# Optimization experiments

Measured on AMD Instinct MI355X. Metric: run time of the kernel, lower is better.

## Reference

```python
import jax, jax.numpy as jnp
import numpy as np

N = 10000; E = 160000; C = 32; NB = 128; H = 64; L = 3; NL = 4; RC = 5.0
DIMS = [1, 3, 5, 7]

def _sph(v):
    # real spherical harmonics l=0..3 of unit vectors v [E,3]
    x, y, z = v[:, 0], v[:, 1], v[:, 2]
    s3 = 3.0 ** 0.5; s5 = 5.0 ** 0.5; s15 = 15.0 ** 0.5; s7 = 7.0 ** 0.5
    sh0 = jnp.ones_like(x)[:, None]
    sh1 = s3 * v
    sh2 = jnp.stack([s15 * x * y, s15 * y * z, (s5 / 2) * (3 * z * z - 1),
                     s15 * x * z, (s15 / 2) * (x * x - y * y)], -1)
    c1 = (35.0 / 8) ** 0.5; c2 = 105.0 ** 0.5; c3 = (21.0 / 8) ** 0.5; c4 = s7 / 2; c5 = (105.0 ** 0.5) / 2
    sh3 = jnp.stack([c1 * y * (3 * x * x - y * y), c2 * x * y * z, c3 * y * (5 * z * z - 1),
                     c4 * (5 * z ** 3 - 3 * z), c3 * x * (5 * z * z - 1),
                     c5 * z * (x * x - y * y), c1 * x * (x * x - 3 * y * y)], -1)
    return [sh0, sh1, sh2, sh3]

def setup_inputs() -> dict:
    key = jax.random.key(0)
    ks = jax.random.split(key, 14)
    inp = {}
    inp['pos'] = jax.random.uniform(ks[0], (N, 3), jnp.float32) * 10.0  # box of side 10
    inp['node_embed'] = jax.random.normal(ks[1], (4, C), jnp.float32)
    inp['rw1'] = jax.random.normal(ks[2], (NB, H), jnp.float32) * 0.1
    inp['rb1'] = jax.random.normal(ks[3], (H,), jnp.float32) * 0.1
    inp['rw2'] = jax.random.normal(ks[4], (H, L * NL * C), jnp.float32) * 0.1
    inp['rb2'] = jax.random.normal(ks[5], (L * NL * C,), jnp.float32) * 0.1
    inp['self_w'] = jax.random.normal(ks[6], (L, NL, C, C), jnp.float32) * (1.0 / C ** 0.5)
    inp['msg_w'] = jax.random.normal(ks[7], (L, NL, C, C), jnp.float32) * (1.0 / C ** 0.5)
    inp['gate_w'] = jax.random.normal(ks[8], (L, C, C), jnp.float32) * (1.0 / C ** 0.5)
    inp['edge_w'] = jax.random.normal(ks[9], (H, NL * C), jnp.float32) * 0.1
    inp['edge_b'] = jax.random.normal(ks[10], (NL * C,), jnp.float32) * 0.1
    inp['species'] = jax.random.randint(ks[11], (N,), 0, 4)
    inp['edge_index'] = jax.random.randint(ks[12], (2, E), 0, N)
    return inp

def reference(pos, node_embed, rw1, rb1, rw2, rb2, self_w, msg_w, gate_w,
              edge_w, edge_b, species, edge_index):
    src, dst = edge_index[0], edge_index[1]
    vec = pos[dst] - pos[src]                       # [E,3]
    r = jnp.sqrt(jnp.sum(vec * vec, -1) + 1e-12)    # [E]
    u = jnp.clip(r / RC, 0.0, 1.0)
    env = 0.5 * (jnp.cos(jnp.pi * u) + 1.0)         # smooth cutoff, 0 beyond rc
    n = jnp.arange(1, NB + 1, dtype=pos.dtype)
    rb = env[:, None] * (2.0 / RC) ** 0.5 * jnp.sin(jnp.pi * n * u[:, None]) / r[:, None]  # Bessel basis [E,NB]
    h = jax.nn.silu(rb @ rw1 + rb1)                 # [E,H]
    w_all = (h @ rw2 + rb2).reshape(E, L, NL, C)    # per-layer per-l radial weights
    ew = (h @ edge_w + edge_b).reshape(E, NL, C)
    sh = _sph(vec / r[:, None])                     # list of [E, 2l+1]
    # node features per l: [N, C, 2l+1]; l=0 initialized from species embedding
    f = [node_embed[species][:, :, None]] + [jnp.zeros((N, C, d), pos.dtype) for d in DIMS[1:]]
    for t in range(L):
        s = f[0][src][:, :, 0]                      # sender scalars [E,C]
        new = []
        for l in range(NL):
            # scalar-gated radial x SH message (equivariant): [E,C,2l+1]
            m = w_all[:, t, l, :, None] * s[:, :, None] * sh[l][:, None, :]
            agg = jax.ops.segment_sum(m, dst, num_segments=N)
            new.append(jnp.einsum('ncm,cd->ndm', f[l], self_w[t, l]) +
                       jnp.einsum('ncm,cd->ndm', agg, msg_w[t, l]))
        gate = jax.nn.sigmoid(new[0][:, :, 0] @ gate_w[t])  # [N,C]
        f = [jax.nn.silu(new[0])] + [new[l] * gate[:, :, None] for l in range(1, NL)]
    node_out = jnp.concatenate([f[l].reshape(N, C * DIMS[l]) for l in range(NL)], -1)   # [N,512]
    g = f[0][src][:, :, 0] + f[0][dst][:, :, 0]     # [E,C]
    edge_out = jnp.concatenate(
        [(ew[:, l, :, None] * g[:, :, None] * sh[l][:, None, :]).reshape(E, C * DIMS[l])
         for l in range(NL)], -1)                   # [E,512]
    return jnp.concatenate([node_out, edge_out], 0)  # [N+E, 512]
```

## Files before the change

### kernel.cpp

```cpp
#include <hip/hip_runtime.h>

#define NN 10000
#define EE 160000
#define CC 32
#define NBAS 128
#define HH 64
#define LL 3
#define ECH 80000

__device__ __forceinline__ float sigmoidf_(float x) { return 1.0f / (1.0f + expf(-x)); }

__device__ __forceinline__ void edge_geom(const float* pos, int src, int dst,
                                          float& inv_r, float& u, float& pref,
                                          float& x, float& y, float& z) {
    float vx = pos[dst * 3 + 0] - pos[src * 3 + 0];
    float vy = pos[dst * 3 + 1] - pos[src * 3 + 1];
    float vz = pos[dst * 3 + 2] - pos[src * 3 + 2];
    float r2 = vx * vx + vy * vy + vz * vz + 1e-12f;
    float r = sqrtf(r2);
    inv_r = 1.0f / r;
    u = fminf(r * 0.2f, 1.0f);
    const float PI = 3.14159265358979f;
    float env = 0.5f * (cosf(PI * u) + 1.0f);
    pref = env * 0.6324555320336759f * inv_r;
    x = vx * inv_r; y = vy * inv_r; z = vz * inv_r;
}

__device__ __forceinline__ void sph_all(float x, float y, float z, float* shv) {
    const float s3 = 1.7320508075688772f, s5 = 2.23606797749979f, s15 = 3.872983346207417f;
    const float c1 = 2.0916500663351885f;
    const float c2 = 10.246950765959598f;
    const float c3 = 1.6201851746019649f;
    const float c4 = 1.3228756555322954f;
    const float c5 = 5.123475382979799f;
    shv[0] = 1.0f;
    shv[1] = s3 * x; shv[2] = s3 * y; shv[3] = s3 * z;
    shv[4] = s15 * x * y;
    shv[5] = s15 * y * z;
    shv[6] = 0.5f * s5 * (3.0f * z * z - 1.0f);
    shv[7] = s15 * x * z;
    shv[8] = 0.5f * s15 * (x * x - y * y);
    shv[9]  = c1 * y * (3.0f * x * x - y * y);
    shv[10] = c2 * x * y * z;
    shv[11] = c3 * y * (5.0f * z * z - 1.0f);
    shv[12] = c4 * (5.0f * z * z * z - 3.0f * z);
    shv[13] = c3 * x * (5.0f * z * z - 1.0f);
    shv[14] = c5 * z * (x * x - y * y);
    shv[15] = c1 * x * (x * x - 3.0f * y * y);
}

__global__ void k_deg(const int* __restrict__ ei, int* __restrict__ deg) {
    int e = blockIdx.x * blockDim.x + threadIdx.x;
    if (e < EE) atomicAdd(&deg[ei[EE + e]], 1);
}

__global__ __launch_bounds__(256) void k_scan(const int* __restrict__ deg, int* __restrict__ rowptr) {
    __shared__ int part[256];
    const int CHUNK = 40;
    int tid = threadIdx.x;
    int s = 0;
#pragma unroll
    for (int k = 0; k < CHUNK; k++) {
        int idx = tid * CHUNK + k;
        if (idx < NN) s += deg[idx];
    }
    part[tid] = s;
    __syncthreads();
    for (int off = 1; off < 256; off <<= 1) {
        int v = (tid >= off) ? part[tid - off] : 0;
        __syncthreads();
        part[tid] += v;
        __syncthreads();
    }
    int run = (tid > 0) ? part[tid - 1] : 0;
#pragma unroll
    for (int k = 0; k < CHUNK; k++) {
        int idx = tid * CHUNK + k;
        if (idx < NN) { rowptr[idx] = run; run += deg[idx]; }
    }
    if (tid == 255) rowptr[NN] = run;
}

__global__ void k_scatter(const int* __restrict__ ei, const int* __restrict__ rowptr,
                          int* __restrict__ cursor, int* __restrict__ csr) {
    int e = blockIdx.x * blockDim.x + threadIdx.x;
    if (e >= EE) return;
    int d = ei[EE + e];
    int slot = atomicAdd(&cursor[d], 1);
    csr[rowptr[d] + slot] = e;
}

__global__ void k_init_f(const float* __restrict__ ne, const int* __restrict__ species,
                         float* __restrict__ f, float* __restrict__ f0) {
    int idx = blockIdx.x * blockDim.x + threadIdx.x;
    if (idx >= NN * CC * 16) return;
    int m = idx & 15;
    int c = (idx >> 4) & 31;
    int n = idx >> 9;
    float v = (m == 0) ? ne[species[n] * CC + c] : 0.0f;
    f[idx] = v;
    if (m == 0) f0[n * CC + c] = v;
}

__global__ __launch_bounds__(256) void k_edge_pre(
    const float* __restrict__ pos, const float* __restrict__ rw1, const float* __restrict__ rb1,
    const int* __restrict__ ei, float* __restrict__ hbuf, float* __restrict__ shbuf) {
    __shared__ float rw1_s[NBAS * HH];
    __shared__ float rb_s[4][NBAS];
    int tid = threadIdx.x;
    for (int i = tid; i < NBAS * HH; i += 256) rw1_s[i] = rw1[i];
    int w = tid >> 6, lane = tid & 63;
    int e = blockIdx.x * 4 + w;
    int src = ei[e], dst = ei[EE + e];
    float inv_r, u, pref, x, y, z;
    edge_geom(pos, src, dst, inv_r, u, pref, x, y, z);
    const float PI = 3.14159265358979f;
#pragma unroll
    for (int rep = 0; rep < 2; rep++) {
        int k = lane + rep * 64;
        rb_s[w][k] = pref * sinf(PI * (float)(k + 1) * u);
    }
    float shv[16];
    sph_all(x, y, z, shv);
    if (lane < 16) {
        float v = shv[0];
#pragma unroll
        for (int k = 1; k < 16; k++) v = (lane == k) ? shv[k] : v;
        shbuf[e * 16 + lane] = v;
    }
    __syncthreads();
    float acc = rb1[lane];
#pragma unroll 8
    for (int n = 0; n < NBAS; n++) acc += rb_s[w][n] * rw1_s[n * HH + lane];
    acc = acc * sigmoidf_(acc);
    hbuf[e * HH + lane] = acc;
}

template<int MODE>
__global__ __launch_bounds__(256) void k_gemm(
    const float* __restrict__ hbuf, const float* __restrict__ W,
    int wstride, int wcol, const float* __restrict__ bias,
    const float* __restrict__ f0, const int* __restrict__ ei,
    const int* __restrict__ csr, float* __restrict__ outw, int ebase) {
    __shared__ float w_s[HH * 128];
    __shared__ float h_s[64][68];
    __shared__ int e_s[64];
    int tid = threadIdx.x;
    int kbase = blockIdx.x * 64 + ebase;
    for (int i = tid; i < HH * 32; i += 256) {
        int j = i >> 5, o4 = (i & 31) << 2;
        *(float4*)&w_s[j * 128 + o4] = *(const float4*)&W[(size_t)j * wstride + wcol + o4];
    }
    {
        int r = tid >> 2, q = tid & 3;
        int p = kbase + r;
        int e = (MODE == 0) ? csr[p] : p;
        if (q == 0) e_s[r] = e;
        const float4* hp = (const float4*)(hbuf + (size_t)e * HH + q * 16);
        float4 v0 = hp[0], v1 = hp[1], v2 = hp[2], v3 = hp[3];
        float4* dp = (float4*)&h_s[r][q * 16];
        dp[0] = v0; dp[1] = v1; dp[2] = v2; dp[3] = v3;
    }
    __syncthreads();
    int ob = (tid & 31) << 2;
    int r0 = (tid >> 5) << 3;
    float acc[8][4];
#pragma unroll
    for (int i = 0; i < 8; i++) { acc[i][0] = 0.f; acc[i][1] = 0.f; acc[i][2] = 0.f; acc[i][3] = 0.f; }
#pragma unroll 2
    for (int k0 = 0; k0 < HH; k0 += 4) {
        float4 w0 = *(float4*)&w_s[(k0 + 0) * 128 + ob];
        float4 w1 = *(float4*)&w_s[(k0 + 1) * 128 + ob];
        float4 w2 = *(float4*)&w_s[(k0 + 2) * 128 + ob];
        float4 w3 = *(float4*)&w_s[(k0 + 3) * 128 + ob];
#pragma unroll
        for (int i = 0; i < 8; i++) {
            float4 hv = *(float4*)&h_s[r0 + i][k0];
            acc[i][0] += hv.x * w0.x; acc[i][1] += hv.x * w0.y; acc[i][2] += hv.x * w0.z; acc[i][3] += hv.x * w0.w;
            acc[i][0] += hv.y * w1.x; acc[i][1] += hv.y * w1.y; acc[i][2] += hv.y * w1.z; acc[i][3] += hv.y * w1.w;
            acc[i][0] += hv.z * w2.x; acc[i][1] += hv.z * w2.y; acc[i][2] += hv.z * w2.z; acc[i][3] += hv.z * w2.w;
            acc[i][0] += hv.w * w3.x; acc[i][1] += hv.w * w3.y; acc[i][2] += hv.w * w3.z; acc[i][3] += hv.w * w3.w;
        }
    }
    float4 bv = *(const float4*)&bias[wcol + ob];
    int cc = ob & 31;
#pragma unroll
    for (int i = 0; i < 8; i++) {
        int rr = r0 + i;
        int e = e_s[rr];
        float4 sc;
        if (MODE == 0) {
            int src = ei[e];
            sc = *(const float4*)&f0[src * CC + cc];
        } else {
            int src = ei[e], dst = ei[EE + e];
            float4 s1 = *(const float4*)&f0[src * CC + cc];
            float4 s2 = *(const float4*)&f0[dst * CC + cc];
            sc.x = s1.x + s2.x; sc.y = s1.y + s2.y; sc.z = s1.z + s2.z; sc.w = s1.w + s2.w;
        }
        float4 res;
        res.x = (acc[i][0] + bv.x) * sc.x;
        res.y = (acc[i][1] + bv.y) * sc.y;
        res.z = (acc[i][2] + bv.z) * sc.z;
        res.w = (acc[i][3] + bv.w) * sc.w;
        size_t prow = (size_t)(kbase - ebase + rr);
        *(float4*)&outw[prow * 128 + ob] = res;
    }
}

__global__ __launch_bounds__(256) void k_agg2(
    const float* __restrict__ aw, const float* __restrict__ shbuf,
    const int* __restrict__ rowptr, const int* __restrict__ csr,
    float* __restrict__ agg) {
    int w = threadIdx.x >> 6, lane = threadIdx.x & 63;
    int n = blockIdx.x * 4 + w;
    int c = lane & 31;
    int half = lane >> 5;
    float acc0[3] = {0.f, 0.f, 0.f};
    float acc1[7] = {0.f, 0.f, 0.f, 0.f, 0.f, 0.f, 0.f};
    int beg = rowptr[n], end = rowptr[n + 1];
    for (int k = beg; k < end; k++) {
        int e = csr[k];
        float a0 = aw[(size_t)k * 128 + lane];
        float a1 = aw[(size_t)k * 128 + 64 + lane];
        const float4* shp = (const float4*)(shbuf + (size_t)e * 16);
        float4 s0 = shp[0], s1 = shp[1], s2 = shp[2], s3 = shp[3];
        if (half == 0) {
            acc0[0] += a0 * s0.x;
            acc1[0] += a1 * s1.x; acc1[1] += a1 * s1.y; acc1[2] += a1 * s1.z; acc1[3] += a1 * s1.w;
            acc1[4] += a1 * s2.x;
        } else {
            acc0[0] += a0 * s0.y; acc0[1] += a0 * s0.z; acc0[2] += a0 * s0.w;
            acc1[0] += a1 * s2.y; acc1[1] += a1 * s2.z; acc1[2] += a1 * s2.w;
            acc1[3] += a1 * s3.x; acc1[4] += a1 * s3.y; acc1[5] += a1 * s3.z; acc1[6] += a1 * s3.w;
        }
    }
    int l0 = half, dl0 = 2 * l0 + 1, mo0 = l0 * l0;
    int l1 = 2 + half, dl1 = 2 * l1 + 1, mo1 = l1 * l1;
    float* ap = agg + ((size_t)n * CC + c) * 16;
#pragma unroll
    for (int m = 0; m < 3; m++)
        if (m < dl0) ap[mo0 + m] = acc0[m];
#pragma unroll
    for (int m = 0; m < 7; m++)
        if (m < dl1) ap[mo1 + m] = acc1[m];
}

__global__ __launch_bounds__(256) void k_node(
    const float* __restrict__ f_cur, const float* __restrict__ agg,
    const float* __restrict__ self_w, const float* __restrict__ msg_w,
    const float* __restrict__ gate_w, float* __restrict__ f_next,
    float* __restrict__ f0_out, int t) {
    __shared__ float new_s[4][CC * 16];
    __shared__ float gate_s[4][CC];
    int w = threadIdx.x >> 6, lane = threadIdx.x & 63;
    int n = blockIdx.x * 4 + w;
    int d = lane & 31, mg = lane >> 5;
#pragma unroll
    for (int k = 0; k < 8; k++) {
        int m = mg + 2 * k;
        int l = (m == 0) ? 0 : (m < 4) ? 1 : (m < 9) ? 2 : 3;
        const float* sw = self_w + (size_t)((t * 4 + l) * CC) * CC + d;
        const float* mw = msg_w + (size_t)((t * 4 + l) * CC) * CC + d;
        const float* fp = f_cur + (size_t)n * CC * 16 + m;
        const float* ap = agg + (size_t)n * CC * 16 + m;
        float acc = 0.0f;
#pragma unroll 8
        for (int c = 0; c < CC; c++)
            acc += fp[c * 16] * sw[c * CC] + ap[c * 16] * mw[c * CC];
        new_s[w][d * 16 + m] = acc;
    }
    __syncthreads();
    if (mg == 0) {
        float g = 0.0f;
#pragma unroll 8
        for (int c = 0; c < CC; c++) g += new_s[w][c * 16 + 0] * gate_w[((size_t)t * CC + c) * CC + d];
        gate_s[w][d] = sigmoidf_(g);
    }
    __syncthreads();
#pragma unroll
    for (int k = 0; k < 8; k++) {
        int m = mg + 2 * k;
        float v = new_s[w][d * 16 + m];
        if (m == 0) v = v * sigmoidf_(v);
        else v *= gate_s[w][d];
        f_next[((size_t)n * CC + d) * 16 + m] = v;
        if (m == 0) f0_out[n * CC + d] = v;
    }
}

__global__ void k_out_node(const float* __restrict__ f, float* __restrict__ out) {
    int idx = blockIdx.x * blockDim.x + threadIdx.x;
    if (idx >= NN * 512) return;
    int n = idx >> 9, q = idx & 511;
    int l, c, m;
    if (q < 32) { l = 0; c = q; m = 0; }
    else if (q < 128) { l = 1; c = (q - 32) / 3; m = (q - 32) % 3; }
    else if (q < 288) { l = 2; c = (q - 128) / 5; m = (q - 128) % 5; }
    else { l = 3; c = (q - 288) / 7; m = (q - 288) % 7; }
    out[idx] = f[((size_t)n * CC + c) * 16 + l * l + m];
}

__global__ __launch_bounds__(256) void k_out_edge2(
    const float* __restrict__ eaw, const float* __restrict__ shbuf,
    float* __restrict__ out, int ebase) {
    int w = threadIdx.x >> 6, lane = threadIdx.x & 63;
    int eloc = blockIdx.x * 4 + w;
    int e = ebase + eloc;
    int c = lane & 31;
    float a0 = eaw[(size_t)eloc * 128 + lane];
    float a1 = eaw[(size_t)eloc * 128 + 64 + lane];
    const float4* shp = (const float4*)(shbuf + (size_t)e * 16);
    float4 s0 = shp[0], s1 = shp[1], s2 = shp[2], s3 = shp[3];
    size_t orow = ((size_t)NN + e) * 512;
    if (lane < 32) {
        out[orow + c] = a0 * s0.x;
        float* op = &out[orow + 128 + c * 5];
        op[0] = a1 * s1.x; op[1] = a1 * s1.y; op[2] = a1 * s1.z; op[3] = a1 * s1.w;
        op[4] = a1 * s2.x;
    } else {
        float* op0 = &out[orow + 32 + c * 3];
        op0[0] = a0 * s0.y; op0[1] = a0 * s0.z; op0[2] = a0 * s0.w;
        float* op1 = &out[orow + 288 + c * 7];
        op1[0] = a1 * s2.y; op1[1] = a1 * s2.z; op1[2] = a1 * s2.w;
        op1[3] = a1 * s3.x; op1[4] = a1 * s3.y; op1[5] = a1 * s3.z; op1[6] = a1 * s3.w;
    }
}

__global__ __launch_bounds__(256) void k_out_edge(
    const float* __restrict__ pos, const float* __restrict__ rw1, const float* __restrict__ rb1,
    const float* __restrict__ edge_w, const float* __restrict__ edge_b,
    const float* __restrict__ f0, const int* __restrict__ ei, float* __restrict__ out) {
    __shared__ float rw1_s[NBAS * HH];
    __shared__ float ew_s[HH * 128];
    __shared__ float rb_s[4][NBAS];
    __shared__ float h_s[4][HH];
    __shared__ float g_s[4][CC];
    __shared__ float sh_s[4][16];
    int tid = threadIdx.x;
    for (int i = tid; i < NBAS * HH; i += 256) rw1_s[i] = rw1[i];
    for (int i = tid; i < HH * 128; i += 256) ew_s[i] = edge_w[i];
    int w = tid >> 6, lane = tid & 63;
    int e = blockIdx.x * 4 + w;
    int src = ei[e], dst = ei[EE + e];
    float inv_r, u, pref, x, y, z;
    edge_geom(pos, src, dst, inv_r, u, pref, x, y, z);
    const float PI = 3.14159265358979f;
#pragma unroll
    for (int rep = 0; rep < 2; rep++) {
        int k = lane + rep * 64;
        rb_s[w][k] = pref * sinf(PI * (float)(k + 1) * u);
    }
    float shv[16];
    sph_all(x, y, z, shv);
    if (lane < 16) {
        float v = shv[0];
#pragma unroll
        for (int k = 1; k < 16; k++) v = (lane == k) ? shv[k] : v;
        sh_s[w][lane] = v;
    }
    if (lane < CC) g_s[w][lane] = f0[src * CC + lane] + f0[dst * CC + lane];
    __syncthreads();
    float acc = rb1[lane];
#pragma unroll 8
    for (int n = 0; n < NBAS; n++) acc += rb_s[w][n] * rw1_s[n * HH + lane];
    h_s[w][lane] = acc * sigmoidf_(acc);
    __syncthreads();
    size_t orow = ((size_t)NN + e) * 512;
#pragma unroll
    for (int rep = 0; rep < 2; rep++) {
        int o = lane + rep * 64;
        int l = o >> 5, c = o & 31;
        float a = edge_b[o];
#pragma unroll 8
        for (int j = 0; j < HH; j++) a += h_s[w][j] * ew_s[j * 128 + o];
        float base = a * g_s[w][c];
        int dl = 2 * l + 1, mo = l * l, co = 32 * l * l;
        for (int m = 0; m < dl; m++) out[orow + co + c * dl + m] = base * sh_s[w][mo + m];
    }
}

extern "C" void kernel_launch(void* const* d_in, const int* in_sizes, int n_in,
                              void* d_out, int out_size, void* d_ws, size_t ws_size,
                              hipStream_t stream) {
    const float* pos        = (const float*)d_in[0];
    const float* node_embed = (const float*)d_in[1];
    const float* rw1        = (const float*)d_in[2];
    const float* rb1        = (const float*)d_in[3];
    const float* rw2        = (const float*)d_in[4];
    const float* rb2        = (const float*)d_in[5];
    const float* self_w     = (const float*)d_in[6];
    const float* msg_w      = (const float*)d_in[7];
    const float* gate_w     = (const float*)d_in[8];
    const float* edge_w     = (const float*)d_in[9];
    const float* edge_b     = (const float*)d_in[10];
    const int* species      = (const int*)d_in[11];
    const int* ei           = (const int*)d_in[12];
    float* out = (float*)d_out;

    float* f0fin = (float*)d_ws;
    float* f0ar  = f0fin + (size_t)NN * CC;
    float* hbuf  = f0ar + (size_t)NN * CC;
    float* shbuf = hbuf + (size_t)EE * HH;
    float* fA    = shbuf + (size_t)EE * 16;
    float* agg   = fA + (size_t)NN * 512;
    int* deg     = (int*)(agg + (size_t)NN * 512);
    int* rowptr  = deg + NN;
    int* cursor  = rowptr + NN + 1;
    int* csr     = cursor + NN;
    size_t base_need = (size_t)((char*)(csr + EE) - (char*)d_ws);
    size_t extra_need = ((size_t)NN * 512 + (size_t)EE * 128) * 4;
    float* fB;
    float* aw;
    bool deep_fallback = false;
    if (ws_size >= base_need + extra_need) {
        fB = (float*)((char*)d_ws + base_need);
        aw = fB + (size_t)NN * 512;
    } else if (ws_size >= base_need) {
        fB = out + (size_t)NN * 512;
        aw = fB + (size_t)NN * 512;
    } else {
        deep_fallback = true;
        float* s = out + (size_t)NN * 512;
        hbuf = s; shbuf = hbuf + (size_t)EE * HH;
        fA = shbuf + (size_t)EE * 16;
        agg = fA + (size_t)NN * 512;
        fB = agg + (size_t)NN * 512;
        aw = fB + (size_t)NN * 512;
        deg = (int*)(aw + (size_t)EE * 128);
        rowptr = deg + NN; cursor = rowptr + NN + 1; csr = cursor + NN;
    }
    float* eaw = fA;

    hipMemsetAsync(deg, 0, (size_t)NN * 4, stream);
    hipMemsetAsync(cursor, 0, (size_t)NN * 4, stream);
    k_deg<<<(EE + 255) / 256, 256, 0, stream>>>(ei, deg);
    k_scan<<<1, 256, 0, stream>>>(deg, rowptr);
    k_scatter<<<(EE + 255) / 256, 256, 0, stream>>>(ei, rowptr, cursor, csr);

    k_init_f<<<(NN * CC * 16 + 255) / 256, 256, 0, stream>>>(node_embed, species, fA, f0ar);
    k_edge_pre<<<EE / 4, 256, 0, stream>>>(pos, rw1, rb1, ei, hbuf, shbuf);

    float* fc = fA;
    float* fn = fB;
    for (int t = 0; t < LL; t++) {
        k_gemm<0><<<EE / 64, 256, 0, stream>>>(hbuf, rw2, 384, t * 128, rb2, f0ar, ei, csr, aw, 0);
        k_agg2<<<NN / 4, 256, 0, stream>>>(aw, shbuf, rowptr, csr, agg);
        float* f0o = (t == LL - 1) ? f0fin : f0ar;
        k_node<<<NN / 4, 256, 0, stream>>>(fc, agg, self_w, msg_w, gate_w, fn, f0o, t);
        float* tmp = fc; fc = fn; fn = tmp;
    }

    k_out_node<<<(NN * 512 + 255) / 256, 256, 0, stream>>>(fc, out);
    if (!deep_fallback) {
        for (int cb = 0; cb < EE; cb += ECH) {
            k_gemm<1><<<ECH / 64, 256, 0, stream>>>(hbuf, edge_w, 128, 0, edge_b, f0fin, ei, csr, eaw, cb);
            k_out_edge2<<<ECH / 4, 256, 0, stream>>>(eaw, shbuf, out, cb);
        }
    } else {
        k_out_edge<<<EE / 4, 256, 0, stream>>>(pos, rw1, rb1, edge_w, edge_b, f0fin, ei, out);
    }
}
```

Before: 1.194 ms.

## Batch radial GEMMs across layers, tile edge MLP, and fuse edge output

The first radial MLP layer becomes a 64-edge tiled GEMM, and the sine basis is computed with a Chebyshev recurrence instead of one sinf per basis term. The per-layer rw2 GEMM is hoisted into a single launch that computes all three layers' weights, which are stored in a wider buffer. The sender-scalar multiply moves into the aggregation kernel. The edge-output GEMM and the spherical-harmonic expansion are fused into one kernel that writes vectorized outputs. This removes repeated weight and hbuf passes and intermediate round trips, at the cost of a larger workspace and extra gather loads in aggregation.

```diff
diff --git a/kernel.cpp b/kernel.cpp
--- a/kernel.cpp
+++ b/kernel.cpp
@@ -6,7 +6,6 @@
 #define NBAS 128
 #define HH 64
 #define LL 3
-#define ECH 80000
 
 __device__ __forceinline__ float sigmoidf_(float x) { return 1.0f / (1.0f + expf(-x)); }
 
@@ -106,112 +105,137 @@
     const float* __restrict__ pos, const float* __restrict__ rw1, const float* __restrict__ rb1,
     const int* __restrict__ ei, float* __restrict__ hbuf, float* __restrict__ shbuf) {
     __shared__ float rw1_s[NBAS * HH];
-    __shared__ float rb_s[4][NBAS];
+    __shared__ float rb_s[64 * 132];
     int tid = threadIdx.x;
-    for (int i = tid; i < NBAS * HH; i += 256) rw1_s[i] = rw1[i];
-    int w = tid >> 6, lane = tid & 63;
-    int e = blockIdx.x * 4 + w;
-    int src = ei[e], dst = ei[EE + e];
-    float inv_r, u, pref, x, y, z;
-    edge_geom(pos, src, dst, inv_r, u, pref, x, y, z);
-    const float PI = 3.14159265358979f;
-#pragma unroll
-    for (int rep = 0; rep < 2; rep++) {
-        int k = lane + rep * 64;
-        rb_s[w][k] = pref * sinf(PI * (float)(k + 1) * u);
-    }
-    float shv[16];
-    sph_all(x, y, z, shv);
-    if (lane < 16) {
-        float v = shv[0];
-#pragma unroll
-        for (int k = 1; k < 16; k++) v = (lane == k) ? shv[k] : v;
-        shbuf[e * 16 + lane] = v;
-    }
-    __syncthreads();
-    float acc = rb1[lane];
-#pragma unroll 8
-    for (int n = 0; n < NBAS; n++) acc += rb_s[w][n] * rw1_s[n * HH + lane];
-    acc = acc * sigmoidf_(acc);
-    hbuf[e * HH + lane] = acc;
-}
-
-template<int MODE>
-__global__ __launch_bounds__(256) void k_gemm(
-    const float* __restrict__ hbuf, const float* __restrict__ W,
-    int wstride, int wcol, const float* __restrict__ bias,
-    const float* __restrict__ f0, const int* __restrict__ ei,
-    const int* __restrict__ csr, float* __restrict__ outw, int ebase) {
+    int ebase = blockIdx.x * 64;
+    for (int i = tid; i < NBAS * HH / 4; i += 256)
+        *(float4*)&rw1_s[i * 4] = *(const float4*)&rw1[i * 4];
+    {
+        int r = tid >> 2, q = tid & 3;
+        int e = ebase + r;
+        int src = ei[e], dst = ei[EE + e];
+        float inv_r, u, pref, x, y, z;
+        edge_geom(pos, src, dst, inv_r, u, pref, x, y, z);
+        float shv[16];
+        sph_all(x, y, z, shv);
+        float4 sv;
+        sv.x = shv[q * 4 + 0]; sv.y = shv[q * 4 + 1];
+        sv.z = shv[q * 4 + 2]; sv.w = shv[q * 4 + 3];
+        *(float4*)&shbuf[(size_t)e * 16 + q * 4] = sv;
+        const float PI = 3.14159265358979f;
+        float th = PI * u;
+        float tc = 2.0f * cosf(th);
+        int n0 = 32 * q + 1;
+        float sp2 = sinf(th * (float)n0);
+        float sp1 = sinf(th * (float)(n0 + 1));
+        float* rp = &rb_s[r * 132 + 32 * q];
+        float4 v;
+        v.x = pref * sp2; v.y = pref * sp1;
+#pragma unroll
+        for (int j = 2; j < 32; j++) {
+            float s = tc * sp1 - sp2;
+            sp2 = sp1; sp1 = s;
+            float pv = pref * s;
+            int m = j & 3;
+            if (m == 0) v.x = pv;
+            else if (m == 1) v.y = pv;
+            else if (m == 2) v.z = pv;
+            else { v.w = pv; *(float4*)&rp[j - 3] = v; }
+        }
+    }
+    __syncthreads();
+    int col0 = (tid & 15) * 4;
+    int r0 = (tid >> 4) * 4;
+    float acc[4][4];
+#pragma unroll
+    for (int i = 0; i < 4; i++) { acc[i][0] = 0.f; acc[i][1] = 0.f; acc[i][2] = 0.f; acc[i][3] = 0.f; }
+#pragma unroll 2
+    for (int k0 = 0; k0 < NBAS; k0 += 4) {
+        float4 w0 = *(float4*)&rw1_s[(k0 + 0) * HH + col0];
+        float4 w1 = *(float4*)&rw1_s[(k0 + 1) * HH + col0];
+        float4 w2 = *(float4*)&rw1_s[(k0 + 2) * HH + col0];
+        float4 w3 = *(float4*)&rw1_s[(k0 + 3) * HH + col0];
+#pragma unroll
+        for (int i = 0; i < 4; i++) {
+            float4 rv = *(float4*)&rb_s[(r0 + i) * 132 + k0];
+            acc[i][0] += rv.x * w0.x; acc[i][1] += rv.x * w0.y; acc[i][2] += rv.x * w0.z; acc[i][3] += rv.x * w0.w;
+            acc[i][0] += rv.y * w1.x; acc[i][1] += rv.y * w1.y; acc[i][2] += rv.y * w1.z; acc[i][3] += rv.y * w1.w;
+            acc[i][0] += rv.z * w2.x; acc[i][1] += rv.z * w2.y; acc[i][2] += rv.z * w2.z; acc[i][3] += rv.z * w2.w;
+            acc[i][0] += rv.w * w3.x; acc[i][1] += rv.w * w3.y; acc[i][2] += rv.w * w3.z; acc[i][3] += rv.w * w3.w;
+        }
+    }
+    float4 bv = *(const float4*)&rb1[col0];
+#pragma unroll
+    for (int i = 0; i < 4; i++) {
+        float a0 = acc[i][0] + bv.x, a1 = acc[i][1] + bv.y;
+        float a2 = acc[i][2] + bv.z, a3 = acc[i][3] + bv.w;
+        float4 hres;
+        hres.x = a0 * sigmoidf_(a0); hres.y = a1 * sigmoidf_(a1);
+        hres.z = a2 * sigmoidf_(a2); hres.w = a3 * sigmoidf_(a3);
+        *(float4*)&hbuf[(size_t)(ebase + r0 + i) * HH + col0] = hres;
+    }
+}
+
+__global__ __launch_bounds__(256) void k_gemm_all(
+    const float* __restrict__ hbuf, const float* __restrict__ rw2,
+    const float* __restrict__ rb2, const int* __restrict__ csr,
+    float* __restrict__ aw, int panel0, int npanel, int ostride) {
     __shared__ float w_s[HH * 128];
     __shared__ float h_s[64][68];
-    __shared__ int e_s[64];
     int tid = threadIdx.x;
-    int kbase = blockIdx.x * 64 + ebase;
-    for (int i = tid; i < HH * 32; i += 256) {
-        int j = i >> 5, o4 = (i & 31) << 2;
-        *(float4*)&w_s[j * 128 + o4] = *(const float4*)&W[(size_t)j * wstride + wcol + o4];
-    }
+    int pbase = blockIdx.x * 64;
     {
         int r = tid >> 2, q = tid & 3;
-        int p = kbase + r;
-        int e = (MODE == 0) ? csr[p] : p;
-        if (q == 0) e_s[r] = e;
+        int e = csr[pbase + r];
         const float4* hp = (const float4*)(hbuf + (size_t)e * HH + q * 16);
         float4 v0 = hp[0], v1 = hp[1], v2 = hp[2], v3 = hp[3];
         float4* dp = (float4*)&h_s[r][q * 16];
         dp[0] = v0; dp[1] = v1; dp[2] = v2; dp[3] = v3;
     }
-    __syncthreads();
     int ob = (tid & 31) << 2;
     int r0 = (tid >> 5) << 3;
-    float acc[8][4];
-#pragma unroll
-    for (int i = 0; i < 8; i++) { acc[i][0] = 0.f; acc[i][1] = 0.f; acc[i][2] = 0.f; acc[i][3] = 0.f; }
+    for (int p = 0; p < npanel; p++) {
+        int wcol = (panel0 + p) * 128;
+        __syncthreads();
+        for (int i = tid; i < HH * 32; i += 256) {
+            int j = i >> 5, o4 = (i & 31) << 2;
+            *(float4*)&w_s[j * 128 + o4] = *(const float4*)&rw2[(size_t)j * 384 + wcol + o4];
+        }
+        __syncthreads();
+        float acc[8][4];
+#pragma unroll
+        for (int i = 0; i < 8; i++) { acc[i][0] = 0.f; acc[i][1] = 0.f; acc[i][2] = 0.f; acc[i][3] = 0.f; }
 #pragma unroll 2
-    for (int k0 = 0; k0 < HH; k0 += 4) {
-        float4 w0 = *(float4*)&w_s[(k0 + 0) * 128 + ob];
-        float4 w1 = *(float4*)&w_s[(k0 + 1) * 128 + ob];
-        float4 w2 = *(float4*)&w_s[(k0 + 2) * 128 + ob];
-        float4 w3 = *(float4*)&w_s[(k0 + 3) * 128 + ob];
+        for (int k0 = 0; k0 < HH; k0 += 4) {
+            float4 w0 = *(float4*)&w_s[(k0 + 0) * 128 + ob];
+            float4 w1 = *(float4*)&w_s[(k0 + 1) * 128 + ob];
+            float4 w2 = *(float4*)&w_s[(k0 + 2) * 128 + ob];
+            float4 w3 = *(float4*)&w_s[(k0 + 3) * 128 + ob];
+#pragma unroll
+            for (int i = 0; i < 8; i++) {
+                float4 hv = *(float4*)&h_s[r0 + i][k0];
+                acc[i][0] += hv.x * w0.x; acc[i][1] += hv.x * w0.y; acc[i][2] += hv.x * w0.z; acc[i][3] += hv.x * w0.w;
+                acc[i][0] += hv.y * w1.x; acc[i][1] += hv.y * w1.y; acc[i][2] += hv.y * w1.z; acc[i][3] += hv.y * w1.w;
+                acc[i][0] += hv.z * w2.x; acc[i][1] += hv.z * w2.y; acc[i][2] += hv.z * w2.z; acc[i][3] += hv.z * w2.w;
+                acc[i][0] += hv.w * w3.x; acc[i][1] += hv.w * w3.y; acc[i][2] += hv.w * w3.z; acc[i][3] += hv.w * w3.w;
+            }
+        }
+        float4 bv = *(const float4*)&rb2[wcol + ob];
 #pragma unroll
         for (int i = 0; i < 8; i++) {
-            float4 hv = *(float4*)&h_s[r0 + i][k0];
-            acc[i][0] += hv.x * w0.x; acc[i][1] += hv.x * w0.y; acc[i][2] += hv.x * w0.z; acc[i][3] += hv.x * w0.w;
-            acc[i][0] += hv.y * w1.x; acc[i][1] += hv.y * w1.y; acc[i][2] += hv.y * w1.z; acc[i][3] += hv.y * w1.w;
-            acc[i][0] += hv.z * w2.x; acc[i][1] += hv.z * w2.y; acc[i][2] += hv.z * w2.z; acc[i][3] += hv.z * w2.w;
-            acc[i][0] += hv.w * w3.x; acc[i][1] += hv.w * w3.y; acc[i][2] += hv.w * w3.z; acc[i][3] += hv.w * w3.w;
-        }
-    }
-    float4 bv = *(const float4*)&bias[wcol + ob];
-    int cc = ob & 31;
-#pragma unroll
-    for (int i = 0; i < 8; i++) {
-        int rr = r0 + i;
-        int e = e_s[rr];
-        float4 sc;
-        if (MODE == 0) {
-            int src = ei[e];
-            sc = *(const float4*)&f0[src * CC + cc];
-        } else {
-            int src = ei[e], dst = ei[EE + e];
-            float4 s1 = *(const float4*)&f0[src * CC + cc];
-            float4 s2 = *(const float4*)&f0[dst * CC + cc];
-            sc.x = s1.x + s2.x; sc.y = s1.y + s2.y; sc.z = s1.z + s2.z; sc.w = s1.w + s2.w;
-        }
-        float4 res;
-        res.x = (acc[i][0] + bv.x) * sc.x;
-        res.y = (acc[i][1] + bv.y) * sc.y;
-        res.z = (acc[i][2] + bv.z) * sc.z;
-        res.w = (acc[i][3] + bv.w) * sc.w;
-        size_t prow = (size_t)(kbase - ebase + rr);
-        *(float4*)&outw[prow * 128 + ob] = res;
+            float4 res;
+            res.x = acc[i][0] + bv.x; res.y = acc[i][1] + bv.y;
+            res.z = acc[i][2] + bv.z; res.w = acc[i][3] + bv.w;
+            *(float4*)&aw[(size_t)(pbase + r0 + i) * ostride + p * 128 + ob] = res;
+        }
     }
 }
 
 __global__ __launch_bounds__(256) void k_agg2(
     const float* __restrict__ aw, const float* __restrict__ shbuf,
+    const float* __restrict__ f0, const int* __restrict__ ei,
     const int* __restrict__ rowptr, const int* __restrict__ csr,
-    float* __restrict__ agg) {
+    float* __restrict__ agg, int coloff, int ostride) {
     int w = threadIdx.x >> 6, lane = threadIdx.x & 63;
     int n = blockIdx.x * 4 + w;
     int c = lane & 31;
@@ -221,8 +245,10 @@
     int beg = rowptr[n], end = rowptr[n + 1];
     for (int k = beg; k < end; k++) {
         int e = csr[k];
-        float a0 = aw[(size_t)k * 128 + lane];
-        float a1 = aw[(size_t)k * 128 + 64 + lane];
+        int src = ei[e];
+        float fs = f0[src * CC + c];
+        float a0 = aw[(size_t)k * ostride + coloff + lane] * fs;
+        float a1 = aw[(size_t)k * ostride + coloff + 64 + lane] * fs;
         const float4* shp = (const float4*)(shbuf + (size_t)e * 16);
         float4 s0 = shp[0], s1 = shp[1], s2 = shp[2], s3 = shp[3];
         if (half == 0) {
@@ -301,29 +327,84 @@
     out[idx] = f[((size_t)n * CC + c) * 16 + l * l + m];
 }
 
-__global__ __launch_bounds__(256) void k_out_edge2(
-    const float* __restrict__ eaw, const float* __restrict__ shbuf,
-    float* __restrict__ out, int ebase) {
-    int w = threadIdx.x >> 6, lane = threadIdx.x & 63;
-    int eloc = blockIdx.x * 4 + w;
-    int e = ebase + eloc;
-    int c = lane & 31;
-    float a0 = eaw[(size_t)eloc * 128 + lane];
-    float a1 = eaw[(size_t)eloc * 128 + 64 + lane];
-    const float4* shp = (const float4*)(shbuf + (size_t)e * 16);
-    float4 s0 = shp[0], s1 = shp[1], s2 = shp[2], s3 = shp[3];
-    size_t orow = ((size_t)NN + e) * 512;
-    if (lane < 32) {
-        out[orow + c] = a0 * s0.x;
-        float* op = &out[orow + 128 + c * 5];
-        op[0] = a1 * s1.x; op[1] = a1 * s1.y; op[2] = a1 * s1.z; op[3] = a1 * s1.w;
-        op[4] = a1 * s2.x;
-    } else {
-        float* op0 = &out[orow + 32 + c * 3];
-        op0[0] = a0 * s0.y; op0[1] = a0 * s0.z; op0[2] = a0 * s0.w;
-        float* op1 = &out[orow + 288 + c * 7];
-        op1[0] = a1 * s2.y; op1[1] = a1 * s2.z; op1[2] = a1 * s2.w;
-        op1[3] = a1 * s3.x; op1[4] = a1 * s3.y; op1[5] = a1 * s3.z; op1[6] = a1 * s3.w;
+template<int DL>
+__device__ __forceinline__ void emit_edge(float* outp, const float* shp,
+                                          float e0, float e1, float e2, float e3) {
+    float ew[4] = {e0, e1, e2, e3};
+    float buf[4 * DL];
+#pragma unroll
+    for (int cc = 0; cc < 4; cc++)
+#pragma unroll
+        for (int m = 0; m < DL; m++) buf[cc * DL + m] = ew[cc] * shp[m];
+#pragma unroll
+    for (int t = 0; t < DL; t++) *(float4*)&outp[t * 4] = *(float4*)&buf[t * 4];
+}
+
+__global__ __launch_bounds__(256) void k_edge_out(
+    const float* __restrict__ hbuf, const float* __restrict__ shbuf,
+    const float* __restrict__ edge_w, const float* __restrict__ edge_b,
+    const float* __restrict__ f0, const int* __restrict__ ei,
+    float* __restrict__ out) {
+    __shared__ float w_s[HH * 128];
+    __shared__ float h_s[64][68];
+    __shared__ float sh_s[64][16];
+    int tid = threadIdx.x;
+    int ebase = blockIdx.x * 64;
+    for (int i = tid; i < HH * 32; i += 256) {
+        int j = i >> 5, o4 = (i & 31) << 2;
+        *(float4*)&w_s[j * 128 + o4] = *(const float4*)&edge_w[(size_t)j * 128 + o4];
+    }
+    {
+        int r = tid >> 2, q = tid & 3;
+        int e = ebase + r;
+        const float4* hp = (const float4*)(hbuf + (size_t)e * HH + q * 16);
+        float4 v0 = hp[0], v1 = hp[1], v2 = hp[2], v3 = hp[3];
+        float4* dp = (float4*)&h_s[r][q * 16];
+        dp[0] = v0; dp[1] = v1; dp[2] = v2; dp[3] = v3;
+        *(float4*)&sh_s[r][q * 4] = *(const float4*)&shbuf[(size_t)e * 16 + q * 4];
+    }
+    __syncthreads();
+    int ob = (tid & 31) << 2;
+    int r0 = (tid >> 5) << 3;
+    float acc[8][4];
+#pragma unroll
+    for (int i = 0; i < 8; i++) { acc[i][0] = 0.f; acc[i][1] = 0.f; acc[i][2] = 0.f; acc[i][3] = 0.f; }
+#pragma unroll 2
+    for (int k0 = 0; k0 < HH; k0 += 4) {
+        float4 w0 = *(float4*)&w_s[(k0 + 0) * 128 + ob];
+        float4 w1 = *(float4*)&w_s[(k0 + 1) * 128 + ob];
+        float4 w2 = *(float4*)&w_s[(k0 + 2) * 128 + ob];
+        float4 w3 = *(float4*)&w_s[(k0 + 3) * 128 + ob];
+#pragma unroll
+        for (int i = 0; i < 8; i++) {
+            float4 hv = *(float4*)&h_s[r0 + i][k0];
+            acc[i][0] += hv.x * w0.x; acc[i][1] += hv.x * w0.y; acc[i][2] += hv.x * w0.z; acc[i][3] += hv.x * w0.w;
+            acc[i][0] += hv.y * w1.x; acc[i][1] += hv.y * w1.y; acc[i][2] += hv.y * w1.z; acc[i][3] += hv.y * w1.w;
+            acc[i][0] += hv.z * w2.x; acc[i][1] += hv.z * w2.y; acc[i][2] += hv.z * w2.z; acc[i][3] += hv.z * w2.w;
+            acc[i][0] += hv.w * w3.x; acc[i][1] += hv.w * w3.y; acc[i][2] += hv.w * w3.z; acc[i][3] += hv.w * w3.w;
+        }
+    }
+    float4 bv = *(const float4*)&edge_b[ob];
+    int l = ob >> 5;
+    int cbase = ob & 31;
+    int dl = 2 * l + 1, mo = l * l, co = 32 * l * l;
+#pragma unroll
+    for (int i = 0; i < 8; i++) {
+        int rr = r0 + i;
+        int e = ebase + rr;
+        int src = ei[e], dst = ei[EE + e];
+        float4 g1 = *(const float4*)&f0[src * CC + cbase];
+        float4 g2 = *(const float4*)&f0[dst * CC + cbase];
+        float e0 = (acc[i][0] + bv.x) * (g1.x + g2.x);
+        float e1 = (acc[i][1] + bv.y) * (g1.y + g2.y);
+        float e2 = (acc[i][2] + bv.z) * (g1.z + g2.z);
+        float e3 = (acc[i][3] + bv.w) * (g1.w + g2.w);
+        float* outp = out + ((size_t)NN + e) * 512 + co + (size_t)cbase * dl;
+        const float* shp = &sh_s[rr][mo];
+        if (l == 0)      emit_edge<1>(outp, shp, e0, e1, e2, e3);
+        else if (l == 1) emit_edge<3>(outp, shp, e0, e1, e2, e3);
+        else if (l == 2) emit_edge<5>(outp, shp, e0, e1, e2, e3);
+        else             emit_edge<7>(outp, shp, e0, e1, e2, e3);
     }
 }
 
@@ -409,7 +490,7 @@
     int* cursor  = rowptr + NN + 1;
     int* csr     = cursor + NN;
     size_t base_need = (size_t)((char*)(csr + EE) - (char*)d_ws);
-    size_t extra_need = ((size_t)NN * 512 + (size_t)EE * 128) * 4;
+    size_t extra_need = ((size_t)NN * 512 + (size_t)EE * 384) * 4;
     float* fB;
     float* aw;
     bool deep_fallback = false;
@@ -430,7 +511,6 @@
         deg = (int*)(aw + (size_t)EE * 128);
         rowptr = deg + NN; cursor = rowptr + NN + 1; csr = cursor + NN;
     }
-    float* eaw = fA;
 
     hipMemsetAsync(deg, 0, (size_t)NN * 4, stream);
     hipMemsetAsync(cursor, 0, (size_t)NN * 4, stream);
@@ -439,25 +519,29 @@
     k_scatter<<<(EE + 255) / 256, 256, 0, stream>>>(ei, rowptr, cursor, csr);
 
     k_init_f<<<(NN * CC * 16 + 255) / 256, 256, 0, stream>>>(node_embed, species, fA, f0ar);
-    k_edge_pre<<<EE / 4, 256, 0, stream>>>(pos, rw1, rb1, ei, hbuf, shbuf);
+    k_edge_pre<<<EE / 64, 256, 0, stream>>>(pos, rw1, rb1, ei, hbuf, shbuf);
 
     float* fc = fA;
     float* fn = fB;
-    for (int t = 0; t < LL; t++) {
-        k_gemm<0><<<EE / 64, 256, 0, stream>>>(hbuf, rw2, 384, t * 128, rb2, f0ar, ei, csr, aw, 0);
-        k_agg2<<<NN / 4, 256, 0, stream>>>(aw, shbuf, rowptr, csr, agg);
-        float* f0o = (t == LL - 1) ? f0fin : f0ar;
-        k_node<<<NN / 4, 256, 0, stream>>>(fc, agg, self_w, msg_w, gate_w, fn, f0o, t);
-        float* tmp = fc; fc = fn; fn = tmp;
-    }
-
-    k_out_node<<<(NN * 512 + 255) / 256, 256, 0, stream>>>(fc, out);
     if (!deep_fallback) {
-        for (int cb = 0; cb < EE; cb += ECH) {
-            k_gemm<1><<<ECH / 64, 256, 0, stream>>>(hbuf, edge_w, 128, 0, edge_b, f0fin, ei, csr, eaw, cb);
-            k_out_edge2<<<ECH / 4, 256, 0, stream>>>(eaw, shbuf, out, cb);
-        }
+        k_gemm_all<<<EE / 64, 256, 0, stream>>>(hbuf, rw2, rb2, csr, aw, 0, 3, 384);
+        for (int t = 0; t < LL; t++) {
+            k_agg2<<<NN / 4, 256, 0, stream>>>(aw, shbuf, f0ar, ei, rowptr, csr, agg, t * 128, 384);
+            float* f0o = (t == LL - 1) ? f0fin : f0ar;
+            k_node<<<NN / 4, 256, 0, stream>>>(fc, agg, self_w, msg_w, gate_w, fn, f0o, t);
+            float* tmp = fc; fc = fn; fn = tmp;
+        }
+        k_out_node<<<(NN * 512 + 255) / 256, 256, 0, stream>>>(fc, out);
+        k_edge_out<<<EE / 64, 256, 0, stream>>>(hbuf, shbuf, edge_w, edge_b, f0fin, ei, out);
     } else {
+        for (int t = 0; t < LL; t++) {
+            k_gemm_all<<<EE / 64, 256, 0, stream>>>(hbuf, rw2, rb2, csr, aw, t, 1, 128);
+            k_agg2<<<NN / 4, 256, 0, stream>>>(aw, shbuf, f0ar, ei, rowptr, csr, agg, 0, 128);
+            float* f0o = (t == LL - 1) ? f0fin : f0ar;
+            k_node<<<NN / 4, 256, 0, stream>>>(fc, agg, self_w, msg_w, gate_w, fn, f0o, t);
+            float* tmp = fc; fc = fn; fn = tmp;
+        }
+        k_out_node<<<(NN * 512 + 255) / 256, 256, 0, stream>>>(fc, out);
         k_out_edge<<<EE / 4, 256, 0, stream>>>(pos, rw1, rb1, edge_w, edge_b, f0fin, ei, out);
     }
 }
```

New measurement: 1.267 ms. 6.2% more time.
